# Kernel optimization log

Measured on AMD Instinct MI355X. Metric: run time of the kernel, lower is better.

The kernel has to match this reference:

```python
import jax, jax.numpy as jnp
import numpy as np

EPS = 1e-08
GROUPS = 128

def log_g(x):
    return jnp.where(x >= 0, jnp.log(jax.nn.relu(x) + 0.5 + EPS), -jax.nn.softplus(-x) + EPS)

def grouped_linear(x, W):
    # x: (B, S, D_in), W: (G, d_out_g, d_in_g) -- grouped 1x1 conv == block-diag linear
    B, S, D = x.shape
    G = W.shape[0]
    xg = x.reshape(B, S, G, D // G)
    y = jnp.einsum('bsgi,goi->bsgo', xg, W)
    return y.reshape(B, S, -1)

def parallel_scan_log(log_coeffs, log_values):
    a_star = jnp.cumsum(log_coeffs + EPS, axis=1)
    log_h0_plus_b_star = jax.lax.cumlogsumexp(log_values - a_star, axis=1)
    return jnp.exp(a_star + log_h0_plus_b_star)

def setup_inputs() -> dict:
    key = jax.random.key(0)
    k_x, k_f, k_i, k_h = jax.random.split(key, 4)
    B, S, D, H = 4, 8192, 1024, 1024
    din_g, dout_g = D // GROUPS, H // GROUPS
    fan_in = din_g  # kernel_size=1
    bound = 1.0 / np.sqrt(fan_in)
    x_t = jax.random.normal(k_x, (B, S, D), dtype=jnp.float32)
    Wf = jax.random.uniform(k_f, (GROUPS, dout_g, din_g), jnp.float32, -bound, bound)
    Wi = jax.random.uniform(k_i, (GROUPS, dout_g, din_g), jnp.float32, -bound, bound)
    Wh = jax.random.uniform(k_h, (GROUPS, dout_g, din_g), jnp.float32, -bound, bound)
    return {"x_t": x_t, "Wf": Wf, "Wi": Wi, "Wh": Wh}

def reference(x_t, Wf, Wi, Wh):
    f_gate = grouped_linear(x_t, Wf)   # (B, S, H)
    i_gate = grouped_linear(x_t, Wi)
    hidden = grouped_linear(x_t, Wh)
    diff = jax.nn.softplus(-f_gate) - jax.nn.softplus(-i_gate)
    log_f = -jax.nn.softplus(diff)
    log_i = -jax.nn.softplus(-diff)
    log_values = log_i + log_g(hidden)  # pre_h is None path
    h_t = parallel_scan_log(log_f, log_values)
    return h_t
```

## Files before the change

### kernel.cpp

```cpp
#include <hip/hip_runtime.h>


constexpr int Bc = 4, Sc = 8192, Dc = 1024, Hc = 1024;
constexpr int CHUNK = 64;
constexpr int HALO  = 32;
constexpr int BLOCK = 256;
constexpr int NCH   = Sc / CHUNK;
constexpr int CQ    = Hc / BLOCK;
constexpr int NBLK  = Bc * CQ * NCH;

__device__ __forceinline__ float frcp(float v) { return __builtin_amdgcn_rcpf(v); }

struct W3 { float wf[8], wi[8], wh[8]; };

__device__ __forceinline__ float step(const float4 x0, const float4 x1,
                                      const W3& w, float h)
{
    const float xr[8] = {x0.x, x0.y, x0.z, x0.w, x1.x, x1.y, x1.z, x1.w};
    float fg = 0.f, ig = 0.f, hh = 0.f;
#pragma unroll
    for (int i = 0; i < 8; ++i) {
        fg = fmaf(xr[i], w.wf[i], fg);
        ig = fmaf(xr[i], w.wi[i], ig);
        hh = fmaf(xr[i], w.wh[i], hh);
    }
    const float Ef = __expf(-fg);
    const float Ei = __expf(-ig);
    const float r  = frcp(2.f + Ef + Ei);
    const float a  = (1.f + Ei) * r;
    const float ic = (1.f + Ef) * r;
    const float gg = (hh >= 0.f) ? (hh + 0.5f) : frcp(1.f + __expf(-hh));
    return fmaf(a, h, ic * gg);
}

__global__ __launch_bounds__(BLOCK, 8)
void minlstm_kernel(const float* __restrict__ x,
                    const float* __restrict__ Wf,
                    const float* __restrict__ Wi,
                    const float* __restrict__ Wh,
                    float* __restrict__ out)
{
    const int blk     = blockIdx.x;
    const int logical = (blk & 7) * (NBLK / 8) + (blk >> 3);
    const int c  = logical & (NCH - 1);
    const int t  = logical / NCH;
    const int cq = t & (CQ - 1);
    const int b  = t / CQ;

    const int hch = cq * BLOCK + (int)threadIdx.x;
    const int g   = hch >> 3;

    W3 w;
    {
        const float* wfp = Wf + (size_t)hch * 8;
        const float* wip = Wi + (size_t)hch * 8;
        const float* whp = Wh + (size_t)hch * 8;
#pragma unroll
        for (int i = 0; i < 8; ++i) { w.wf[i] = wfp[i]; w.wi[i] = wip[i]; w.wh[i] = whp[i]; }
    }

    const int warm = (c != 0) ? HALO : 0;
    const int s0   = c * CHUNK;
    const int nit  = warm + CHUNK;

    const float* xp = x + ((size_t)b * Sc + (s0 - warm)) * Dc + g * 8;
    float* op = out + ((size_t)(b * Sc + (s0 - warm)) * Hc) + hch;

    float h = 0.f;

    float4 nx0 = *(const float4*)(xp);
    float4 nx1 = *(const float4*)(xp + 4);
    xp += Dc;

#pragma unroll 4
    for (int s = 0; s < nit; ++s) {
        const float4 x0 = nx0;
        const float4 x1 = nx1;
        if (s + 1 < nit) {
            nx0 = *(const float4*)(xp);
            nx1 = *(const float4*)(xp + 4);
            xp += Dc;
        }
        h = step(x0, x1, w, h);
        if (s >= warm)
            __builtin_nontemporal_store(h, op);
        op += Hc;
    }
}

extern "C" void kernel_launch(void* const* d_in, const int* in_sizes, int n_in,
                              void* d_out, int out_size, void* d_ws, size_t ws_size,
                              hipStream_t stream) {
    (void)in_sizes; (void)n_in; (void)d_ws; (void)ws_size; (void)out_size;
    minlstm_kernel<<<dim3(NBLK), dim3(BLOCK), 0, stream>>>(
        (const float*)d_in[0], (const float*)d_in[1],
        (const float*)d_in[2], (const float*)d_in[3], (float*)d_out);
}
```

Before: 291.0 us.

## Stage x rows into LDS via async global_load_lds with 4-slot ring pipeline

```diff
diff --git a/kernel.cpp b/kernel.cpp
--- a/kernel.cpp
+++ b/kernel.cpp
@@ -5,32 +5,25 @@
 constexpr int CHUNK = 64;
 constexpr int HALO  = 32;
 constexpr int BLOCK = 256;
+constexpr int WAVES = BLOCK / 64;
 constexpr int NCH   = Sc / CHUNK;
 constexpr int CQ    = Hc / BLOCK;
 constexpr int NBLK  = Bc * CQ * NCH;
 
 __device__ __forceinline__ float frcp(float v) { return __builtin_amdgcn_rcpf(v); }
 
-struct W3 { float wf[8], wi[8], wh[8]; };
+#define GLOAD_LDS16(gp, lp)                                                      \
+    __builtin_amdgcn_global_load_lds(                                            \
+        (const __attribute__((address_space(1))) void*)(gp),                     \
+        (__attribute__((address_space(3))) void*)(lp), 16, 0, 0)
 
-__device__ __forceinline__ float step(const float4 x0, const float4 x1,
-                                      const W3& w, float h)
+__device__ __forceinline__ float dot8(float4 a0, float4 a1, float4 b0, float4 b1)
 {
-    const float xr[8] = {x0.x, x0.y, x0.z, x0.w, x1.x, x1.y, x1.z, x1.w};
-    float fg = 0.f, ig = 0.f, hh = 0.f;
-#pragma unroll
-    for (int i = 0; i < 8; ++i) {
-        fg = fmaf(xr[i], w.wf[i], fg);
-        ig = fmaf(xr[i], w.wi[i], ig);
-        hh = fmaf(xr[i], w.wh[i], hh);
-    }
-    const float Ef = __expf(-fg);
-    const float Ei = __expf(-ig);
-    const float r  = frcp(2.f + Ef + Ei);
-    const float a  = (1.f + Ei) * r;
-    const float ic = (1.f + Ef) * r;
-    const float gg = (hh >= 0.f) ? (hh + 0.5f) : frcp(1.f + __expf(-hh));
-    return fmaf(a, h, ic * gg);
+    float s = a0.x * b0.x;
+    s = fmaf(a0.y, b0.y, s); s = fmaf(a0.z, b0.z, s); s = fmaf(a0.w, b0.w, s);
+    s = fmaf(a1.x, b1.x, s); s = fmaf(a1.y, b1.y, s);
+    s = fmaf(a1.z, b1.z, s); s = fmaf(a1.w, b1.w, s);
+    return s;
 }
 
 __global__ __launch_bounds__(BLOCK, 8)
@@ -40,6 +33,8 @@
                     const float* __restrict__ Wh,
                     float* __restrict__ out)
 {
+    __shared__ float smem[WAVES * 1024];
+
     const int blk     = blockIdx.x;
     const int logical = (blk & 7) * (NBLK / 8) + (blk >> 3);
     const int c  = logical & (NCH - 1);
@@ -47,45 +42,84 @@
     const int cq = t & (CQ - 1);
     const int b  = t / CQ;
 
-    const int hch = cq * BLOCK + (int)threadIdx.x;
-    const int g   = hch >> 3;
+    const int tid  = (int)threadIdx.x;
+    const int lane = tid & 63;
+    const int w    = tid >> 6;
+    const int hch  = cq * BLOCK + tid;
 
-    W3 w;
-    {
-        const float* wfp = Wf + (size_t)hch * 8;
-        const float* wip = Wi + (size_t)hch * 8;
-        const float* whp = Wh + (size_t)hch * 8;
-#pragma unroll
-        for (int i = 0; i < 8; ++i) { w.wf[i] = wfp[i]; w.wi[i] = wip[i]; w.wh[i] = whp[i]; }
-    }
+    const float4* wfp = (const float4*)(Wf + (size_t)hch * 8);
+    const float4* wip = (const float4*)(Wi + (size_t)hch * 8);
+    const float4* whp = (const float4*)(Wh + (size_t)hch * 8);
+    const float4 wf0 = wfp[0], wf1 = wfp[1];
+    const float4 wi0 = wip[0], wi1 = wip[1];
+    const float4 wh0 = whp[0], wh1 = whp[1];
 
-    const int warm = (c != 0) ? HALO : 0;
-    const int s0   = c * CHUNK;
-    const int nit  = warm + CHUNK;
+    const int warm  = (c != 0) ? HALO : 0;
+    const int s0    = c * CHUNK;
+    const int srow0 = s0 - warm;
+    const int NG    = (warm + CHUNK) >> 2;
+    const int NGw   = warm >> 2;
 
-    const float* xp = x + ((size_t)b * Sc + (s0 - warm)) * Dc + g * 8;
-    float* op = out + ((size_t)(b * Sc + (s0 - warm)) * Hc) + hch;
+    const int colf = cq * 256 + w * 64;
+    const float* gstage = x + ((size_t)(b * Sc + srow0 + (lane >> 4)) * Dc)
+                            + colf + (lane & 15) * 4;
+
+    float* const wslice = smem + w * 1024;
+    const int lxo = (lane >> 3) * 8;
+
+    float* const op = out + (size_t)(b * Sc + srow0) * Hc + hch;
 
     float h = 0.f;
 
-    float4 nx0 = *(const float4*)(xp);
-    float4 nx1 = *(const float4*)(xp + 4);
-    xp += Dc;
+    auto stage = [&](int slot) {
+        GLOAD_LDS16(gstage, wslice + slot * 256);
+        gstage += (size_t)4 * Dc;
+    };
+    auto compute_group = [&](int gq, bool do_store) {
+        const float* rp = wslice + (gq & 3) * 256 + lxo;
+#pragma unroll
+        for (int r = 0; r < 4; ++r) {
+            const float4 x0 = *(const float4*)(rp + r * 64);
+            const float4 x1 = *(const float4*)(rp + r * 64 + 4);
+            const float fg = dot8(x0, x1, wf0, wf1);
+            const float ig = dot8(x0, x1, wi0, wi1);
+            const float hh = dot8(x0, x1, wh0, wh1);
+            const float Ef = __expf(-fg);
+            const float Ei = __expf(-ig);
+            const float rd = frcp(2.f + Ef + Ei);
+            const float a  = (1.f + Ei) * rd;
+            const float ic = 1.f - a;
+            const float gg = (hh >= 0.f) ? (hh + 0.5f)
+                                         : frcp(1.f + __expf(-hh));
+            h = fmaf(a, h, ic * gg);
+            if (do_store)
+                __builtin_nontemporal_store(h, op + (size_t)(gq * 4 + r) * Hc);
+        }
+    };
 
-#pragma unroll 4
-    for (int s = 0; s < nit; ++s) {
-        const float4 x0 = nx0;
-        const float4 x1 = nx1;
-        if (s + 1 < nit) {
-            nx0 = *(const float4*)(xp);
-            nx1 = *(const float4*)(xp + 4);
-            xp += Dc;
-        }
-        h = step(x0, x1, w, h);
-        if (s >= warm)
-            __builtin_nontemporal_store(h, op);
-        op += Hc;
+    stage(0); stage(1); stage(2);
+
+    int gq = 0;
+    for (; gq < NGw; ++gq) {
+        stage((gq + 3) & 3);
+        asm volatile("s_waitcnt vmcnt(3)" ::: "memory");
+        compute_group(gq, false);
     }
+    stage((gq + 3) & 3);
+    asm volatile("s_waitcnt vmcnt(3)" ::: "memory");
+    compute_group(gq, true);
+    ++gq;
+    for (; gq < NG - 3; ++gq) {
+        stage((gq + 3) & 3);
+        asm volatile("s_waitcnt vmcnt(7)" ::: "memory");
+        compute_group(gq, true);
+    }
+    asm volatile("s_waitcnt vmcnt(6)" ::: "memory");
+    compute_group(gq, true); ++gq;
+    asm volatile("s_waitcnt vmcnt(5)" ::: "memory");
+    compute_group(gq, true); ++gq;
+    asm volatile("s_waitcnt vmcnt(4)" ::: "memory");
+    compute_group(gq, true);
 }
 
 extern "C" void kernel_launch(void* const* d_in, const int* in_sizes, int n_in,
```

Result: faster. 266.0 us (-8.6%).
